# Optimization experiments

Hardware: AMD Instinct MI355X
Metric: run time of the kernel (lower is better)

Reference implementation:

```python
import jax, jax.numpy as jnp
import numpy as np

GAMMA = 0.5          # blending coeff from __init__
NEG_SLOPE = 0.2      # LeakyReLU slope
MASK_FILL = -9e15    # zero_vec constant from source

N, M, D = 8192, 8192, 256
SPARSITY = 0.01


def setup_inputs() -> dict:
    key = jax.random.key(0)
    k1, k2, k3, k4, k5 = jax.random.split(key, 5)
    input1 = jax.random.normal(k1, (N, D), dtype=jnp.float32)
    input2 = jax.random.normal(k2, (M, D), dtype=jnp.float32)
    adj = (jax.random.uniform(k3, (N, M)) < SPARSITY).astype(jnp.float32)
    # xavier_normal with gain=1.414 on (D,1): std = gain*sqrt(2/(D+1))
    std = 1.414 * np.sqrt(2.0 / (D + 1))
    a1 = jax.random.normal(k4, (D, 1), dtype=jnp.float32) * std
    a2 = jax.random.normal(k5, (D, 1), dtype=jnp.float32) * std
    return {"input1": input1, "input2": input2, "adj": adj, "a1": a1, "a2": a2}


def reference(input1, input2, adj, a1, a2):
    # e1: (N,1) broadcast against e2: (1,M) -> e: (N,M)
    e1 = input1 @ a1                      # (N,1)
    e2 = (input2 @ a2).T                  # (1,M)
    e = jax.nn.leaky_relu(e1 + e2, negative_slope=NEG_SLOPE)
    attention = jnp.where(adj > 0, e, MASK_FILL)
    attention = jax.nn.softmax(attention, axis=1)
    # scale each row by its adjacency degree, then gamma-blend with adj
    attention = attention * jnp.sum(adj, axis=1, keepdims=True)
    attention = attention * GAMMA + adj * (1.0 - GAMMA)
    return attention @ input2             # (N,D)
```

## Files before the change

### kernel.cpp

```cpp
#include <hip/hip_runtime.h>
#include <cstdint>
#include <cstddef>

#define NEG_SLOPE 0.2f
#define CAP 160

typedef float f32x4 __attribute__((ext_vector_type(4)));
typedef unsigned short u16x4 __attribute__((ext_vector_type(4)));

static __device__ __forceinline__ unsigned short f2bf_rne(float f) {
  unsigned u = __float_as_uint(f);
  unsigned r = (u + 0x7FFFu + ((u >> 16) & 1u)) >> 16;
  return (unsigned short)r;
}
static __device__ __forceinline__ float bf2f(unsigned short h) {
  return __uint_as_float((unsigned)h << 16);
}

__global__ __launch_bounds__(256) void score_conv_kernel(
    const float* __restrict__ x1, const float* __restrict__ x2,
    const float* __restrict__ a1, const float* __restrict__ a2,
    float* __restrict__ e1, unsigned short* __restrict__ f2h,
    unsigned short* __restrict__ x2h, int N, int M, int D) {
  int gtid = blockIdx.x * blockDim.x + threadIdx.x;
  int wid = gtid >> 6;
  int lane = threadIdx.x & 63;
  if (wid >= N + M) return;
  const float4 av = *reinterpret_cast<const float4*>(
      ((wid < N) ? a1 : a2) + lane * 4);
  if (wid < N) {
    const float4 xv = *reinterpret_cast<const float4*>(x1 + (size_t)wid * D + lane * 4);
    float s = xv.x * av.x + xv.y * av.y + xv.z * av.z + xv.w * av.w;
    #pragma unroll
    for (int off = 32; off > 0; off >>= 1) s += __shfl_down(s, off, 64);
    if (lane == 0) e1[wid] = s;
  } else {
    int row = wid - N;
    const float4 xv = *reinterpret_cast<const float4*>(x2 + (size_t)row * D + lane * 4);
    float s = xv.x * av.x + xv.y * av.y + xv.z * av.z + xv.w * av.w;
    u16x4 h;
    h.x = f2bf_rne(xv.x); h.y = f2bf_rne(xv.y);
    h.z = f2bf_rne(xv.z); h.w = f2bf_rne(xv.w);
    reinterpret_cast<u16x4*>(x2h)[(size_t)row * (D >> 2) + lane] = h;
    #pragma unroll
    for (int off = 32; off > 0; off >>= 1) s += __shfl_down(s, off, 64);
    if (lane == 0) f2h[row] = f2bf_rne(s);
  }
}

__global__ __launch_bounds__(256) void attn_kernel(
    const float* __restrict__ adj, const unsigned short* __restrict__ x2h,
    const float* __restrict__ e1, const unsigned short* __restrict__ f2h,
    float* __restrict__ out, int N, int M, int D) {
  __shared__ unsigned short s_f2h[8192];
  __shared__ int   s_idx[4][CAP];
  __shared__ float s_w[4][CAP];

  const int tid  = threadIdx.x;
  const int wv   = tid >> 6;
  const int lane = tid & 63;
  const int row  = blockIdx.x * 4 + wv;

  {
    const u16x4* src = reinterpret_cast<const u16x4*>(f2h);
    u16x4* dst = reinterpret_cast<u16x4*>(s_f2h);
    #pragma unroll
    for (int i = 0; i < 8; ++i) dst[tid + i * 256] = src[tid + i * 256];
  }
  __syncthreads();
  if (row >= N) return;

  const int D4 = D >> 2;
  const float e1i = e1[row];
  const f32x4* __restrict__ arow4 =
      reinterpret_cast<const f32x4*>(adj + (size_t)row * M);

  uint64_t m0 = 0ull, m1 = 0ull;
  #pragma unroll 8
  for (int it = 0; it < 16; ++it) {
    f32x4 v = __builtin_nontemporal_load(&arow4[it * 64 + lane]);
    uint64_t b = 0;
    if (v.x > 0.f) b |= 1ull;
    if (v.y > 0.f) b |= 2ull;
    if (v.z > 0.f) b |= 4ull;
    if (v.w > 0.f) b |= 8ull;
    m0 |= b << (it * 4);
  }
  #pragma unroll 8
  for (int it = 16; it < 32; ++it) {
    f32x4 v = __builtin_nontemporal_load(&arow4[it * 64 + lane]);
    uint64_t b = 0;
    if (v.x > 0.f) b |= 1ull;
    if (v.y > 0.f) b |= 2ull;
    if (v.z > 0.f) b |= 4ull;
    if (v.w > 0.f) b |= 8ull;
    m1 |= b << ((it - 16) * 4);
  }
  const int cnt = __popcll(m0) + __popcll(m1);

  int incl = cnt;
  #pragma unroll
  for (int off = 1; off < 64; off <<= 1) {
    int t = __shfl_up(incl, off, 64);
    if (lane >= off) incl += t;
  }
  int pos = incl - cnt;
  const int K = __shfl(incl, 63, 64);

  while (m0) {
    int b = __ffsll((unsigned long long)m0) - 1;
    m0 &= m0 - 1;
    int j = ((((b >> 2) << 6) + lane) << 2) + (b & 3);
    float e = e1i + bf2f(s_f2h[j]);
    e = (e > 0.f) ? e : NEG_SLOPE * e;
    if (pos < CAP) { s_idx[wv][pos] = j; s_w[wv][pos] = e; }
    ++pos;
  }
  while (m1) {
    int b = __ffsll((unsigned long long)m1) - 1;
    m1 &= m1 - 1;
    int j = (((((b >> 2) + 16) << 6) + lane) << 2) + (b & 3);
    float e = e1i + bf2f(s_f2h[j]);
    e = (e > 0.f) ? e : NEG_SLOPE * e;
    if (pos < CAP) { s_idx[wv][pos] = j; s_w[wv][pos] = e; }
    ++pos;
  }

  f32x4* __restrict__ out4 = reinterpret_cast<f32x4*>(out);
  if (K == 0) {
    f32x4 z; z.x = z.y = z.z = z.w = 0.f;
    __builtin_nontemporal_store(z, &out4[(size_t)row * D4 + lane]);
    return;
  }

  const int Kc = (K < CAP) ? K : CAP;
  float lm = -1e30f;
  for (int k = lane; k < Kc; k += 64) lm = fmaxf(lm, s_w[wv][k]);
  #pragma unroll
  for (int off = 32; off > 0; off >>= 1) lm = fmaxf(lm, __shfl_xor(lm, off, 64));
  float ls = 0.f;
  for (int k = lane; k < Kc; k += 64) {
    float pr = __expf(s_w[wv][k] - lm);
    s_w[wv][k] = pr;
    ls += pr;
  }
  #pragma unroll
  for (int off = 32; off > 0; off >>= 1) ls += __shfl_xor(ls, off, 64);
  const float scale = 0.5f * (float)K / ls;
  for (int k = lane; k < Kc; k += 64) s_w[wv][k] = s_w[wv][k] * scale + 0.5f;

  const u16x4* __restrict__ x2h4 = reinterpret_cast<const u16x4*>(x2h);
  float4 a0, a1v, a2v, a3;
  a0.x = a0.y = a0.z = a0.w = 0.f; a1v = a0; a2v = a0; a3 = a0;
  int k = 0;
  for (; k + 4 <= Kc; k += 4) {
    int j0 = __builtin_amdgcn_readfirstlane(s_idx[wv][k + 0]);
    int j1 = __builtin_amdgcn_readfirstlane(s_idx[wv][k + 1]);
    int j2 = __builtin_amdgcn_readfirstlane(s_idx[wv][k + 2]);
    int j3 = __builtin_amdgcn_readfirstlane(s_idx[wv][k + 3]);
    float w0 = s_w[wv][k + 0], w1 = s_w[wv][k + 1];
    float w2 = s_w[wv][k + 2], w3 = s_w[wv][k + 3];
    u16x4 h0 = x2h4[(size_t)j0 * D4 + lane];
    u16x4 h1 = x2h4[(size_t)j1 * D4 + lane];
    u16x4 h2 = x2h4[(size_t)j2 * D4 + lane];
    u16x4 h3 = x2h4[(size_t)j3 * D4 + lane];
    a0.x = fmaf(w0, bf2f(h0.x), a0.x); a0.y = fmaf(w0, bf2f(h0.y), a0.y);
    a0.z = fmaf(w0, bf2f(h0.z), a0.z); a0.w = fmaf(w0, bf2f(h0.w), a0.w);
    a1v.x = fmaf(w1, bf2f(h1.x), a1v.x); a1v.y = fmaf(w1, bf2f(h1.y), a1v.y);
    a1v.z = fmaf(w1, bf2f(h1.z), a1v.z); a1v.w = fmaf(w1, bf2f(h1.w), a1v.w);
    a2v.x = fmaf(w2, bf2f(h2.x), a2v.x); a2v.y = fmaf(w2, bf2f(h2.y), a2v.y);
    a2v.z = fmaf(w2, bf2f(h2.z), a2v.z); a2v.w = fmaf(w2, bf2f(h2.w), a2v.w);
    a3.x = fmaf(w3, bf2f(h3.x), a3.x); a3.y = fmaf(w3, bf2f(h3.y), a3.y);
    a3.z = fmaf(w3, bf2f(h3.z), a3.z); a3.w = fmaf(w3, bf2f(h3.w), a3.w);
  }
  for (; k < Kc; ++k) {
    int j = __builtin_amdgcn_readfirstlane(s_idx[wv][k]);
    float w = s_w[wv][k];
    u16x4 h = x2h4[(size_t)j * D4 + lane];
    a0.x = fmaf(w, bf2f(h.x), a0.x); a0.y = fmaf(w, bf2f(h.y), a0.y);
    a0.z = fmaf(w, bf2f(h.z), a0.z); a0.w = fmaf(w, bf2f(h.w), a0.w);
  }
  f32x4 r;
  r.x = (a0.x + a1v.x) + (a2v.x + a3.x);
  r.y = (a0.y + a1v.y) + (a2v.y + a3.y);
  r.z = (a0.z + a1v.z) + (a2v.z + a3.z);
  r.w = (a0.w + a1v.w) + (a2v.w + a3.w);
  __builtin_nontemporal_store(r, &out4[(size_t)row * D4 + lane]);
}

extern "C" void kernel_launch(void* const* d_in, const int* in_sizes, int n_in,
                              void* d_out, int out_size, void* d_ws, size_t ws_size,
                              hipStream_t stream) {
  const float* x1  = (const float*)d_in[0];
  const float* x2  = (const float*)d_in[1];
  const float* adj = (const float*)d_in[2];
  const float* a1  = (const float*)d_in[3];
  const float* a2  = (const float*)d_in[4];
  float* out = (float*)d_out;

  const int D = in_sizes[3];
  const int N = in_sizes[0] / D;
  const int M = in_sizes[1] / D;

  char* p = (char*)d_ws;
  float* e1 = (float*)p;                    p += (size_t)N * 4;
  unsigned short* f2h = (unsigned short*)p; p += (size_t)M * 2;
  unsigned short* x2h = (unsigned short*)p;

  const int waves = N + M;
  const int blocks1 = (waves * 64 + 255) / 256;
  score_conv_kernel<<<blocks1, 256, 0, stream>>>(x1, x2, a1, a2, e1, f2h, x2h, N, M, D);
  attn_kernel<<<(N + 3) / 4, 256, 0, stream>>>(adj, x2h, e1, f2h, out, N, M, D);
}
```

Measured before the change: 76.72 us.

## Split adjacency bitmask compression into separate kernel and keep f2 in fp32

```diff
diff --git a/kernel.cpp b/kernel.cpp
--- a/kernel.cpp
+++ b/kernel.cpp
@@ -7,6 +7,8 @@
 
 typedef float f32x4 __attribute__((ext_vector_type(4)));
 typedef unsigned short u16x4 __attribute__((ext_vector_type(4)));
+typedef unsigned long long u64;
+typedef u64 u64x2 __attribute__((ext_vector_type(2)));
 
 static __device__ __forceinline__ unsigned short f2bf_rne(float f) {
   unsigned u = __float_as_uint(f);
@@ -20,7 +22,7 @@
 __global__ __launch_bounds__(256) void score_conv_kernel(
     const float* __restrict__ x1, const float* __restrict__ x2,
     const float* __restrict__ a1, const float* __restrict__ a2,
-    float* __restrict__ e1, unsigned short* __restrict__ f2h,
+    float* __restrict__ e1, float* __restrict__ f2,
     unsigned short* __restrict__ x2h, int N, int M, int D) {
   int gtid = blockIdx.x * blockDim.x + threadIdx.x;
   int wid = gtid >> 6;
@@ -44,37 +46,17 @@
     reinterpret_cast<u16x4*>(x2h)[(size_t)row * (D >> 2) + lane] = h;
     #pragma unroll
     for (int off = 32; off > 0; off >>= 1) s += __shfl_down(s, off, 64);
-    if (lane == 0) f2h[row] = f2bf_rne(s);
-  }
-}
-
-__global__ __launch_bounds__(256) void attn_kernel(
-    const float* __restrict__ adj, const unsigned short* __restrict__ x2h,
-    const float* __restrict__ e1, const unsigned short* __restrict__ f2h,
-    float* __restrict__ out, int N, int M, int D) {
-  __shared__ unsigned short s_f2h[8192];
-  __shared__ int   s_idx[4][CAP];
-  __shared__ float s_w[4][CAP];
-
-  const int tid  = threadIdx.x;
-  const int wv   = tid >> 6;
-  const int lane = tid & 63;
-  const int row  = blockIdx.x * 4 + wv;
-
-  {
-    const u16x4* src = reinterpret_cast<const u16x4*>(f2h);
-    u16x4* dst = reinterpret_cast<u16x4*>(s_f2h);
-    #pragma unroll
-    for (int i = 0; i < 8; ++i) dst[tid + i * 256] = src[tid + i * 256];
-  }
-  __syncthreads();
-  if (row >= N) return;
-
-  const int D4 = D >> 2;
-  const float e1i = e1[row];
+    if (lane == 0) f2[row] = s;
+  }
+}
+
+__global__ __launch_bounds__(256) void compress_kernel(
+    const float* __restrict__ adj, u64* __restrict__ mask, int N, int M) {
+  const int wid  = (blockIdx.x * blockDim.x + threadIdx.x) >> 6;
+  const int lane = threadIdx.x & 63;
+  if (wid >= N) return;
   const f32x4* __restrict__ arow4 =
-      reinterpret_cast<const f32x4*>(adj + (size_t)row * M);
-
+      reinterpret_cast<const f32x4*>(adj + (size_t)wid * M);
   uint64_t m0 = 0ull, m1 = 0ull;
   #pragma unroll 8
   for (int it = 0; it < 16; ++it) {
@@ -96,6 +78,37 @@
     if (v.w > 0.f) b |= 8ull;
     m1 |= b << ((it - 16) * 4);
   }
+  u64x2 w; w.x = m0; w.y = m1;
+  reinterpret_cast<u64x2*>(mask)[(size_t)wid * 64 + lane] = w;
+}
+
+__global__ __launch_bounds__(256) void attn_lite_kernel(
+    const u64* __restrict__ mask, const unsigned short* __restrict__ x2h,
+    const float* __restrict__ e1, const float* __restrict__ f2,
+    float* __restrict__ out, int N, int M, int D) {
+  __shared__ float s_f2[8192];
+  __shared__ int   s_idx[4][CAP];
+  __shared__ float s_w[4][CAP];
+
+  const int tid  = threadIdx.x;
+  const int wv   = tid >> 6;
+  const int lane = tid & 63;
+  const int row  = blockIdx.x * 4 + wv;
+
+  {
+    const f32x4* src = reinterpret_cast<const f32x4*>(f2);
+    f32x4* dst = reinterpret_cast<f32x4*>(s_f2);
+    #pragma unroll
+    for (int i = 0; i < 8; ++i) dst[tid + i * 256] = src[tid + i * 256];
+  }
+  __syncthreads();
+  if (row >= N) return;
+
+  const int D4 = D >> 2;
+  const float e1i = e1[row];
+
+  u64x2 mm = reinterpret_cast<const u64x2*>(mask)[(size_t)row * 64 + lane];
+  uint64_t m0 = mm.x, m1 = mm.y;
   const int cnt = __popcll(m0) + __popcll(m1);
 
   int incl = cnt;
@@ -111,7 +124,7 @@
     int b = __ffsll((unsigned long long)m0) - 1;
     m0 &= m0 - 1;
     int j = ((((b >> 2) << 6) + lane) << 2) + (b & 3);
-    float e = e1i + bf2f(s_f2h[j]);
+    float e = e1i + s_f2[j];
     e = (e > 0.f) ? e : NEG_SLOPE * e;
     if (pos < CAP) { s_idx[wv][pos] = j; s_w[wv][pos] = e; }
     ++pos;
@@ -120,7 +133,7 @@
     int b = __ffsll((unsigned long long)m1) - 1;
     m1 &= m1 - 1;
     int j = (((((b >> 2) + 16) << 6) + lane) << 2) + (b & 3);
-    float e = e1i + bf2f(s_f2h[j]);
+    float e = e1i + s_f2[j];
     e = (e > 0.f) ? e : NEG_SLOPE * e;
     if (pos < CAP) { s_idx[wv][pos] = j; s_w[wv][pos] = e; }
     ++pos;
@@ -204,11 +217,13 @@
 
   char* p = (char*)d_ws;
   float* e1 = (float*)p;                    p += (size_t)N * 4;
-  unsigned short* f2h = (unsigned short*)p; p += (size_t)M * 2;
-  unsigned short* x2h = (unsigned short*)p;
+  float* f2 = (float*)p;                    p += (size_t)M * 4;
+  unsigned short* x2h = (unsigned short*)p; p += (size_t)M * D * 2;
+  u64* mask = (u64*)p;
 
   const int waves = N + M;
   const int blocks1 = (waves * 64 + 255) / 256;
-  score_conv_kernel<<<blocks1, 256, 0, stream>>>(x1, x2, a1, a2, e1, f2h, x2h, N, M, D);
-  attn_kernel<<<(N + 3) / 4, 256, 0, stream>>>(adj, x2h, e1, f2h, out, N, M, D);
-}
+  score_conv_kernel<<<blocks1, 256, 0, stream>>>(x1, x2, a1, a2, e1, f2, x2h, N, M, D);
+  compress_kernel<<<(N + 3) / 4, 256, 0, stream>>>(adj, mask, N, M);
+  attn_lite_kernel<<<(N + 3) / 4, 256, 0, stream>>>(mask, x2h, e1, f2, out, N, M, D);
+}
```

New measurement: 87.53 us. +14.1%, slower.
